# Kernel optimization log

Measured on AMD Instinct MI355X. Metric: run time of the kernel, lower is better.

Reference implementation:

```python
import jax, jax.numpy as jnp
import numpy as np

BN_EPS = 1e-5

def _l2norm(x):
    n = jnp.sqrt(jnp.sum(x * x, axis=-1, keepdims=True))
    return x / jnp.maximum(n, 1e-12)

def _bn_eval(x, gamma, beta):
    # eval-mode BatchNorm2d (running_mean=0, running_var=1)
    g = gamma / jnp.sqrt(1.0 + BN_EPS)
    return x * g[None, :, None, None] + beta[None, :, None, None]

def _forward(feat, Wq, Wk, Wv, ad_conv_w, ad_conv_b, pm_w1, pm_w2,
             back_w, catt, catt1, mlp_w, mlp_b, mlp_gamma, mlp_beta,
             dsn_w, dsn_b, dsn_gamma, dsn_beta):
    B, C, H, W = feat.shape
    p = pm_w1.shape[1]  # p_num (top-k size)
    x2d = feat.reshape(B, C, H * W).transpose(0, 2, 1)          # [B,HW,C]
    q = jnp.einsum('bnc,dc->bnd', x2d, Wq)                       # [B,HW,cim]
    k = jnp.einsum('bnc,dc->bnd', x2d, Wk)
    v = jnp.einsum('bnc,dc->bnd', x2d, Wv)
    # cosine-similarity attention weights [B,HW,HW]
    w = jnp.einsum('bid,bjd->bij', _l2norm(q), _l2norm(k))
    wv, idx = jax.lax.top_k(w, p)                                # [B,HW,p]
    vg = jax.vmap(lambda vv, ii: vv[ii])(v, idx)                 # [B,HW,p,cim] gather
    # ADConv: 1x1 conv on a single channel == scalar affine
    xa = wv * ad_conv_w[0] + ad_conv_b[0]
    pos = jnp.where(xa > 0, xa, 0.0)
    hdn = jax.nn.relu(jnp.einsum('bip,qp->biq', pos, pm_w1))     # [B,HW,2p]
    mask = jax.nn.sigmoid(jnp.einsum('biq,pq->bip', hdn, pm_w2)) # [B,HW,p]
    att = jax.nn.softmax(jnp.where(xa > 0, xa, -100000.0), axis=-1)
    wfin = att * mask                                            # [B,HW,p]
    ov = jnp.einsum('bip,bipd->bid', wfin, vg)                   # [B,HW,cim]
    ov = jnp.einsum('bid,cd->bic', ov, back_w)                   # [B,HW,C]
    v_img = catt * ov.transpose(0, 2, 1).reshape(B, C, H, W)
    cat = jnp.concatenate([v_img, catt1 * feat], axis=1)         # [B,2C,H,W]
    x = jnp.einsum('oc,bchw->bohw', mlp_w, cat) + mlp_b[None, :, None, None]
    x = jax.nn.relu(_bn_eval(x, mlp_gamma, mlp_beta))
    r0 = jnp.einsum('oc,bchw->bohw', dsn_w, x) + dsn_b[None, :, None, None]
    r0 = jax.nn.relu(_bn_eval(r0, dsn_gamma, dsn_beta))
    return x, r0

def setup_inputs() -> dict:
    key = jax.random.key(0)
    ks = jax.random.split(key, 12)
    B, C, H, W = 2, 256, 80, 80
    cim, p = C // 8, 9
    sc = 0.05
    return {
        'feat': jax.random.normal(ks[0], (B, C, H, W), jnp.float32),
        'Wq': jax.random.normal(ks[1], (cim, C), jnp.float32) * sc,
        'Wk': jax.random.normal(ks[2], (cim, C), jnp.float32) * sc,
        'Wv': jax.random.normal(ks[3], (cim, C), jnp.float32) * sc,
        'ad_conv_w': jnp.ones((1,), jnp.float32),
        'ad_conv_b': jnp.zeros((1,), jnp.float32),
        'pm_w1': jax.random.normal(ks[4], (2 * p, p), jnp.float32) * 0.3,
        'pm_w2': jax.random.normal(ks[5], (p, 2 * p), jnp.float32) * 0.3,
        'back_w': jax.random.normal(ks[6], (C, cim), jnp.float32) * sc,
        'catt': jnp.ones((1, C, 1, 1), jnp.float32),
        'catt1': jnp.ones((1, C, 1, 1), jnp.float32),
        'mlp_w': jax.random.normal(ks[7], (C, 2 * C), jnp.float32) * sc,
        'mlp_b': jnp.zeros((C,), jnp.float32),
        'mlp_gamma': jnp.ones((C,), jnp.float32),
        'mlp_beta': jnp.zeros((C,), jnp.float32),
        'dsn_w': jax.random.normal(ks[8], (1, C), jnp.float32) * sc,
        'dsn_b': jnp.zeros((1,), jnp.float32),
        'dsn_gamma': jnp.ones((1,), jnp.float32),
        'dsn_beta': jnp.zeros((1,), jnp.float32),
        'H': H,
        'W': W,
    }

def reference(feat, Wq, Wk, Wv, ad_conv_w, ad_conv_b, pm_w1, pm_w2,
              back_w, catt, catt1, mlp_w, mlp_b, mlp_gamma, mlp_beta,
              dsn_w, dsn_b, dsn_gamma, dsn_beta, H, W):
    # H,W < 768 -> get_forward branch
    return _forward(feat, Wq, Wk, Wv, ad_conv_w, ad_conv_b, pm_w1, pm_w2,
                    back_w, catt, catt1, mlp_w, mlp_b, mlp_gamma, mlp_beta,
                    dsn_w, dsn_b, dsn_gamma, dsn_beta)
```

## Files before the change

kernel.cpp:

```cpp
#include <hip/hip_runtime.h>
#include <hip/hip_bf16.h>

#define HW   6400
#define NB   2
#define CC   256
#define CIM  32
#define PP   9
#define P2   18
#define ROWS (NB*HW)
#define NCH  32
#define JCH  (HW/NCH)
#define NCHF 64
#define JCHF (HW/NCHF)
#define NGRP (ROWS/64)
#define CAPR 256

typedef float f4 __attribute__((ext_vector_type(4)));

#define OFF_QN   0
#define OFF_KN   (OFF_QN + ROWS*CIM)
#define OFF_V    (OFF_KN + ROWS*CIM)
#define OFF_OV   (OFF_V  + ROWS*CIM)
#define OFF_PV   (OFF_OV + ROWS*CIM)
#define OFF_PI   (OFF_PV + ROWS*NCH*PP)
#define OFF_W1T  (OFF_PI + ROWS*NCH*PP)
#define OFF_W2T  (OFF_W1T + CIM*CC)
#define OFF_BF   (OFF_W2T + CC*CC)
#define OFF_WQT  (OFF_BF + CC)
#define OFF_WKT  (OFF_WQT + CC*CIM)
#define OFF_WVT  (OFF_WKT + CC*CIM)
#define OFF_TH   (OFF_WVT + CC*CIM)
#define OFF_SC   (OFF_TH + ROWS)
#define OFF_SV   OFF_PV

__global__ void prep_kernel(const float* __restrict__ mlp_w, const float* __restrict__ mlp_b,
                            const float* __restrict__ mlp_g, const float* __restrict__ mlp_be,
                            const float* __restrict__ back_w, const float* __restrict__ catt,
                            const float* __restrict__ catt1,
                            const float* __restrict__ Wq, const float* __restrict__ Wk,
                            const float* __restrict__ Wv, float* __restrict__ ws) {
    const int blk = blockIdx.x, t = threadIdx.x;
    const float bnc = rsqrtf(1.0f + 1e-5f);
    if (blk < 32) {
        const int d = blk, o = t;
        const float g = mlp_g[o] * bnc;
        float acc = 0.f;
        for (int c = 0; c < CC; ++c)
            acc = fmaf(mlp_w[o*512 + c] * catt[c], back_w[c*CIM + d], acc);
        ws[OFF_W1T + d*CC + o] = g * acc;
    } else if (blk == 32) {
        const int o = t;
        const float g = mlp_g[o] * bnc;
        for (int c = 0; c < CC; ++c)
            ws[OFF_W2T + c*CC + o] = g * mlp_w[o*512 + 256 + c] * catt1[c];
        ws[OFF_BF + o] = g * mlp_b[o] + mlp_be[o];
    } else {
        const float* W = (blk == 33) ? Wq : (blk == 34) ? Wk : Wv;
        float* WT = ws + ((blk == 33) ? OFF_WQT : (blk == 34) ? OFF_WKT : OFF_WVT);
        for (int i = t; i < CC*CIM; i += 256) {
            const int c = i / CIM, d = i % CIM;
            WT[c*CIM + d] = W[d*CC + c];
        }
    }
}

__global__ __launch_bounds__(256) void qkv_kernel(const float* __restrict__ feat,
                                                  const float* __restrict__ ws_r,
                                                  float* __restrict__ ws) {
    __shared__ float part[4][64][33];
    __shared__ float invA[64];
    const int bx = blockIdx.x;
    const int mat = bx % 3;
    const int ng  = bx / 3;
    const int n0  = ng * 64;
    const int b   = n0 / HW;
    const int nsp0 = n0 % HW;
    const int tid = threadIdx.x;
    const int w = __builtin_amdgcn_readfirstlane(tid >> 6);
    const int lane = tid & 63;
    const float* WT = ws_r + (mat == 0 ? OFF_WQT : mat == 1 ? OFF_WKT : OFF_WVT);
    const float* fbase = feat + (size_t)b*CC*HW + nsp0 + lane;
    float acc[CIM];
#pragma unroll
    for (int d = 0; d < CIM; ++d) acc[d] = 0.f;
    const int c0 = w * 64;
    for (int cc = 0; cc < 64; cc += 2) {
        const int c = c0 + cc;
        const float fv0 = fbase[(size_t)c * HW];
        const float fv1 = fbase[(size_t)(c+1) * HW];
        const float* wt0 = WT + c*CIM;
        const float* wt1 = wt0 + CIM;
#pragma unroll
        for (int d = 0; d < CIM; ++d) acc[d] = fmaf(fv0, wt0[d], acc[d]);
#pragma unroll
        for (int d = 0; d < CIM; ++d) acc[d] = fmaf(fv1, wt1[d], acc[d]);
    }
#pragma unroll
    for (int d = 0; d < CIM; ++d) part[w][lane][d] = acc[d];
    __syncthreads();
    {
        const int n = tid >> 2, d0 = (tid & 3) * 8;
#pragma unroll
        for (int dd = 0; dd < 8; ++dd) {
            const int d = d0 + dd;
            part[0][n][d] = part[0][n][d] + part[1][n][d] + part[2][n][d] + part[3][n][d];
        }
    }
    __syncthreads();
    if (mat < 2) {
        if (tid < 64) {
            const int n = tid;
            float ss = 0.f;
#pragma unroll
            for (int d = 0; d < CIM; ++d) { const float x = part[0][n][d]; ss = fmaf(x, x, ss); }
            invA[n] = 1.0f / fmaxf(sqrtf(ss), 1e-12f);
        }
        __syncthreads();
    }
    float* outp = ws + (mat == 0 ? OFF_QN : mat == 1 ? OFF_KN : OFF_V);
    {
        const int n = tid >> 2, d0 = (tid & 3) * 8;
        const float scl = (mat < 2) ? invA[n] : 1.0f;
        const size_t r = (size_t)(n0 + n);
#pragma unroll
        for (int dd = 0; dd < 8; ++dd)
            outp[r*CIM + d0 + dd] = part[0][n][d0 + dd] * scl;
    }
}

__global__ __launch_bounds__(256) void attn_sample(const float* __restrict__ ws_r,
                                                   float* __restrict__ ws) {
    const int tid  = threadIdx.x;
    const int wid  = (blockIdx.x << 2) + (tid >> 6);
    const int lane = tid & 63;
    const int rg = __builtin_amdgcn_readfirstlane(wid >> 5);
    const int ch = __builtin_amdgcn_readfirstlane(wid & (NCH-1));
    const int r = rg*64 + lane;
    const int b = (rg*64) / HW;
    const float* qn = ws_r + OFF_QN + (size_t)r*CIM;
    float q[CIM];
    {   const f4* qv = (const f4*)qn;
        f4* q4 = (f4*)q;
#pragma unroll
        for (int h = 0; h < 8; ++h) q4[h] = qv[h];
    }
    const float* kbase = ws_r + OFF_KN + ((size_t)b*HW + ch*JCH)*CIM;
    const int jbase = ch*JCH;
    float tv[PP]; int ti[PP];
#pragma unroll
    for (int s = 0; s < PP; ++s) { tv[s] = -3.0e38f; ti[s] = 0; }
    for (int j = 0; j < JCH; j += 8) {
        const float* kp = kbase + j*CIM;
        float a0 = 0.f, a1 = 0.f, a2 = 0.f, a3 = 0.f;
#pragma unroll
        for (int d = 0; d < CIM; d += 4) {
            a0 = fmaf(q[d+0], kp[d+0], a0);
            a1 = fmaf(q[d+1], kp[d+1], a1);
            a2 = fmaf(q[d+2], kp[d+2], a2);
            a3 = fmaf(q[d+3], kp[d+3], a3);
        }
        const float wv = (a0 + a1) + (a2 + a3);
        if (wv > tv[8]) {
            tv[8] = wv; ti[8] = jbase + j;
#pragma unroll
            for (int s = 8; s > 0; --s) {
                const bool sw = tv[s] > tv[s-1];
                const float vA = tv[s-1], vB = tv[s];
                tv[s-1] = sw ? vB : vA;  tv[s] = sw ? vA : vB;
                const int iA = ti[s-1], iB = ti[s];
                ti[s-1] = sw ? iB : iA;  ti[s] = sw ? iA : iB;
            }
        }
    }
    float* pv = ws + OFF_PV + ((size_t)r*NCH + ch)*PP;
    int*   pi = (int*)(ws + OFF_PI) + ((size_t)r*NCH + ch)*PP;
#pragma unroll
    for (int s = 0; s < PP; ++s) { pv[s] = tv[s]; pi[s] = ti[s]; }
}

#define NSLOT 5
__global__ __launch_bounds__(256) void theta_kernel(const float* __restrict__ ws_r,
                                                    float* __restrict__ ws) {
    const int tid = threadIdx.x;
    const int w = tid >> 6, lane = tid & 63;
    const int r = blockIdx.x*4 + w;
    const float* pv = ws_r + OFF_PV + (size_t)r*NCH*PP;
    const int*   pi = (const int*)(ws_r + OFF_PI) + (size_t)r*NCH*PP;
    float cv[NSLOT]; int ci[NSLOT];
#pragma unroll
    for (int i = 0; i < NSLOT; ++i) {
        const int s = lane + 64*i;
        if (s < NCH*PP) { cv[i] = pv[s]; ci[i] = pi[s]; }
        else            { cv[i] = -3e38f; ci[i] = 0x7fffffff; }
    }
    float s9 = -3e38f;
#pragma unroll
    for (int rd = 0; rd < PP; ++rd) {
        float hv = cv[0]; int hi = ci[0]; int hs = 0;
#pragma unroll
        for (int i = 1; i < NSLOT; ++i)
            if (cv[i] > hv || (cv[i] == hv && ci[i] < hi)) { hv = cv[i]; hi = ci[i]; hs = i; }
        float bv = hv; int bi = hi;
#pragma unroll
        for (int off = 32; off >= 1; off >>= 1) {
            const float ov_ = __shfl_xor(bv, off);
            const int   oi_ = __shfl_xor(bi, off);
            if (ov_ > bv || (ov_ == bv && oi_ < bi)) { bv = ov_; bi = oi_; }
        }
        const bool won = (hv == bv && hi == bi);
#pragma unroll
        for (int i = 0; i < NSLOT; ++i)
            if (won && i == hs) cv[i] = -3e38f;
        s9 = bv;
    }
    if (lane == 0) {
        ws[OFF_TH + r] = s9;
        ((int*)(ws + OFF_SC))[r] = 0;
    }
}

__global__ __launch_bounds__(256) void attn_filter(const float* __restrict__ ws_r,
                                                   float* __restrict__ ws) {
    const int tid  = threadIdx.x;
    const int wid  = (blockIdx.x << 2) + (tid >> 6);
    const int lane = tid & 63;
    const int rg = __builtin_amdgcn_readfirstlane(wid >> 6);
    const int ch = __builtin_amdgcn_readfirstlane(wid & (NCHF-1));
    const int r = rg*64 + lane;
    const int b = (rg*64) / HW;
    const float* qn = ws_r + OFF_QN + (size_t)r*CIM;
    float q[CIM];
    {   const f4* qv = (const f4*)qn;
        f4* q4 = (f4*)q;
#pragma unroll
        for (int h = 0; h < 8; ++h) q4[h] = qv[h];
    }
    const float th = ws_r[OFF_TH + r];
    int* sc = (int*)(ws + OFF_SC);
    float* sv = ws + OFF_SV;
    const float* kbase = ws_r + OFF_KN + ((size_t)b*HW + ch*JCHF)*CIM;
    const int jbase = ch*JCHF;
#pragma unroll 2
    for (int j = 0; j < JCHF; ++j) {
        const float* kp = kbase + j*CIM;
        float a0 = 0.f, a1 = 0.f, a2 = 0.f, a3 = 0.f;
#pragma unroll
        for (int d = 0; d < CIM; d += 4) {
            a0 = fmaf(q[d+0], kp[d+0], a0);
            a1 = fmaf(q[d+1], kp[d+1], a1);
            a2 = fmaf(q[d+2], kp[d+2], a2);
            a3 = fmaf(q[d+3], kp[d+3], a3);
        }
        const float wv = (a0 + a1) + (a2 + a3);
        if (wv >= th) {
            const int slot = atomicAdd(&sc[r], 1);
            if (slot < CAPR) {
                float2 pr;
                pr.x = wv;
                pr.y = __int_as_float(jbase + j);
                *(float2*)(sv + ((size_t)r*CAPR + slot)*2) = pr;
            }
        }
    }
}

#define NS2 4
__global__ __launch_bounds__(256) void merge2_kernel(const float* __restrict__ ws_r,
                                                     const float* __restrict__ pm_w1,
                                                     const float* __restrict__ pm_w2,
                                                     const float* __restrict__ ad_w,
                                                     const float* __restrict__ ad_b,
                                                     float* __restrict__ ws) {
    __shared__ float pm1[P2*PP];
    __shared__ float pm2[PP*P2];
    const int tid = threadIdx.x;
    for (int i = tid; i < P2*PP; i += 256) pm1[i] = pm_w1[i];
    for (int i = tid; i < PP*P2; i += 256) pm2[i] = pm_w2[i];
    __syncthreads();
    const int w = tid >> 6, lane = tid & 63;
    const int r = blockIdx.x*4 + w;
    const int b = r / HW;
    const int cnt0 = ((const int*)(ws_r + OFF_SC))[r];
    const int cnl = cnt0 < CAPR ? cnt0 : CAPR;
    const float* svp = ws_r + OFF_SV + (size_t)r*CAPR*2;
    float cv[NS2]; int ci[NS2];
#pragma unroll
    for (int i = 0; i < NS2; ++i) {
        const int s = lane + 64*i;
        if (s < cnl) {
            const float2 pr = *(const float2*)(svp + (size_t)s*2);
            cv[i] = pr.x; ci[i] = __float_as_int(pr.y);
        } else { cv[i] = -3e38f; ci[i] = 0x7fffffff; }
    }
    float topv[PP]; int topi[PP];
#pragma unroll
    for (int rd = 0; rd < PP; ++rd) {
        float hv = cv[0]; int hi = ci[0]; int hs = 0;
#pragma unroll
        for (int i = 1; i < NS2; ++i)
            if (cv[i] > hv || (cv[i] == hv && ci[i] < hi)) { hv = cv[i]; hi = ci[i]; hs = i; }
        float bv = hv; int bi = hi;
#pragma unroll
        for (int off = 32; off >= 1; off >>= 1) {
            const float ov_ = __shfl_xor(bv, off);
            const int   oi_ = __shfl_xor(bi, off);
            if (ov_ > bv || (ov_ == bv && oi_ < bi)) { bv = ov_; bi = oi_; }
        }
        const bool won = (hv == bv && hi == bi);
#pragma unroll
        for (int i = 0; i < NS2; ++i)
            if (won && i == hs) cv[i] = -3e38f;
        topv[rd] = bv;
        topi[rd] = (bi >= 0 && bi < HW) ? bi : 0;
    }
    const float adw = ad_w[0], adb = ad_b[0];
    float xa[PP], pos[PP];
#pragma unroll
    for (int p = 0; p < PP; ++p) { xa[p] = fmaf(topv[p], adw, adb); pos[p] = fmaxf(xa[p], 0.f); }
    float hdn[P2];
#pragma unroll
    for (int qq = 0; qq < P2; ++qq) {
        float a = 0.f;
#pragma unroll
        for (int p = 0; p < PP; ++p) a = fmaf(pos[p], pm1[qq*PP + p], a);
        hdn[qq] = fmaxf(a, 0.f);
    }
    float msk[PP];
#pragma unroll
    for (int p = 0; p < PP; ++p) {
        float a = 0.f;
#pragma unroll
        for (int qq = 0; qq < P2; ++qq) a = fmaf(hdn[qq], pm2[p*P2 + qq], a);
        msk[p] = 1.0f / (1.0f + expf(-a));
    }
    float xm[PP], m = -3e38f;
#pragma unroll
    for (int p = 0; p < PP; ++p) { xm[p] = xa[p] > 0.f ? xa[p] : -100000.0f; m = fmaxf(m, xm[p]); }
    float e[PP], ssum = 0.f;
#pragma unroll
    for (int p = 0; p < PP; ++p) { e[p] = expf(xm[p] - m); ssum += e[p]; }
    float wf[PP];
#pragma unroll
    for (int p = 0; p < PP; ++p) wf[p] = (e[p] / ssum) * msk[p];
    const int d = lane & 31;
    const float* vb = ws_r + OFF_V + (size_t)b*HW*CIM;
    float acc = 0.f;
#pragma unroll
    for (int p = 0; p < PP; ++p) acc = fmaf(wf[p], vb[(size_t)topi[p]*CIM + d], acc);
    if (lane < 32) ws[OFF_OV + (size_t)r*CIM + d] = acc;
}

__global__ __launch_bounds__(64) void fin_kernel(const float* __restrict__ feat,
                                                 const float* __restrict__ ws_r,
                                                 float* __restrict__ out) {
    __shared__ float ovt[64*33];
    const int bx = blockIdx.x;
    const int ng = bx % NGRP;
    const int og = bx / NGRP;
    const int n0 = ng*64;
    const int b  = n0 / HW;
    const int nsp0 = n0 % HW;
    const int lane = threadIdx.x;
    const float4* ovg = (const float4*)(ws_r + OFF_OV + (size_t)n0*CIM);
#pragma unroll
    for (int i = 0; i < 8; ++i) {
        const int f = lane + 64*i;
        const float4 vv = ovg[f];
        const int row = f >> 3, col = (f & 7) * 4;
        ovt[row*33 + col]     = vv.x;
        ovt[row*33 + col + 1] = vv.y;
        ovt[row*33 + col + 2] = vv.z;
        ovt[row*33 + col + 3] = vv.w;
    }
    __syncthreads();
    const int o0 = og * 16;
    float acc[16];
    const float* bfp = ws_r + OFF_BF;
#pragma unroll
    for (int oi = 0; oi < 16; ++oi) acc[oi] = bfp[o0 + oi];
    const float* w1t = ws_r + OFF_W1T;
    for (int dd = 0; dd < CIM; dd += 4) {
        const float xv0 = ovt[lane*33 + dd+0];
        const float xv1 = ovt[lane*33 + dd+1];
        const float xv2 = ovt[lane*33 + dd+2];
        const float xv3 = ovt[lane*33 + dd+3];
        const float* w0 = w1t + (dd+0)*CC + o0;
        const float* w1 = w1t + (dd+1)*CC + o0;
        const float* w2 = w1t + (dd+2)*CC + o0;
        const float* w3 = w1t + (dd+3)*CC + o0;
#pragma unroll
        for (int oi = 0; oi < 16; ++oi) acc[oi] = fmaf(xv0, w0[oi], acc[oi]);
#pragma unroll
        for (int oi = 0; oi < 16; ++oi) acc[oi] = fmaf(xv1, w1[oi], acc[oi]);
#pragma unroll
        for (int oi = 0; oi < 16; ++oi) acc[oi] = fmaf(xv2, w2[oi], acc[oi]);
#pragma unroll
        for (int oi = 0; oi < 16; ++oi) acc[oi] = fmaf(xv3, w3[oi], acc[oi]);
    }
    const float* w2t = ws_r + OFF_W2T;
    const float* fbase = feat + (size_t)b*CC*HW + nsp0 + lane;
    for (int c = 0; c < CC; c += 4) {
        const float fv0 = fbase[(size_t)(c+0) * HW];
        const float fv1 = fbase[(size_t)(c+1) * HW];
        const float fv2 = fbase[(size_t)(c+2) * HW];
        const float fv3 = fbase[(size_t)(c+3) * HW];
        const float* w0 = w2t + (c+0)*CC + o0;
        const float* w1 = w2t + (c+1)*CC + o0;
        const float* w2 = w2t + (c+2)*CC + o0;
        const float* w3 = w2t + (c+3)*CC + o0;
#pragma unroll
        for (int oi = 0; oi < 16; ++oi) acc[oi] = fmaf(fv0, w0[oi], acc[oi]);
#pragma unroll
        for (int oi = 0; oi < 16; ++oi) acc[oi] = fmaf(fv1, w1[oi], acc[oi]);
#pragma unroll
        for (int oi = 0; oi < 16; ++oi) acc[oi] = fmaf(fv2, w2[oi], acc[oi]);
#pragma unroll
        for (int oi = 0; oi < 16; ++oi) acc[oi] = fmaf(fv3, w3[oi], acc[oi]);
    }
    const size_t obase = (size_t)b*CC*HW + nsp0 + lane;
#pragma unroll
    for (int oi = 0; oi < 16; ++oi)
        out[obase + (size_t)(o0 + oi)*HW] = fmaxf(acc[oi], 0.f);
}

__global__ __launch_bounds__(256) void dsn_kernel(const float* __restrict__ xout,
                                                  const float* __restrict__ dsn_w,
                                                  const float* __restrict__ dsn_b,
                                                  const float* __restrict__ dsn_g,
                                                  const float* __restrict__ dsn_be,
                                                  float* __restrict__ out) {
    const int t = blockIdx.x*256 + threadIdx.x;
    const int b = t / HW, nsp = t % HW;
    const float* xb = xout + (size_t)b*CC*HW + nsp;
    float acc = 0.f;
#pragma unroll 4
    for (int o = 0; o < CC; ++o)
        acc = fmaf(xb[(size_t)o*HW], dsn_w[o], acc);
    const float g = dsn_g[0] * rsqrtf(1.0f + 1e-5f);
    const float r0 = fmaxf(fmaf(g, acc + dsn_b[0], dsn_be[0]), 0.f);
    out[(size_t)NB*CC*HW + t] = r0;
}

extern "C" void kernel_launch(void* const* d_in, const int* in_sizes, int n_in,
                              void* d_out, int out_size, void* d_ws, size_t ws_size,
                              hipStream_t stream) {
    const float* feat  = (const float*)d_in[0];
    const float* Wq    = (const float*)d_in[1];
    const float* Wk    = (const float*)d_in[2];
    const float* Wv    = (const float*)d_in[3];
    const float* adw   = (const float*)d_in[4];
    const float* adb   = (const float*)d_in[5];
    const float* pm_w1 = (const float*)d_in[6];
    const float* pm_w2 = (const float*)d_in[7];
    const float* backw = (const float*)d_in[8];
    const float* catt  = (const float*)d_in[9];
    const float* catt1 = (const float*)d_in[10];
    const float* mlp_w = (const float*)d_in[11];
    const float* mlp_b = (const float*)d_in[12];
    const float* mlp_g = (const float*)d_in[13];
    const float* mlp_be= (const float*)d_in[14];
    const float* dsn_w = (const float*)d_in[15];
    const float* dsn_b = (const float*)d_in[16];
    const float* dsn_g = (const float*)d_in[17];
    const float* dsn_be= (const float*)d_in[18];
    float* ws = (float*)d_ws;
    float* out = (float*)d_out;

    prep_kernel<<<36, 256, 0, stream>>>(mlp_w, mlp_b, mlp_g, mlp_be, backw, catt, catt1,
                                        Wq, Wk, Wv, ws);
    qkv_kernel<<<NGRP*3, 256, 0, stream>>>(feat, ws, ws);
    attn_sample<<<(NGRP*NCH)/4, 256, 0, stream>>>(ws, ws);
    theta_kernel<<<ROWS/4, 256, 0, stream>>>(ws, ws);
    attn_filter<<<(NGRP*NCHF)/4, 256, 0, stream>>>(ws, ws);
    merge2_kernel<<<ROWS/4, 256, 0, stream>>>(ws, pm_w1, pm_w2, adw, adb, ws);
    fin_kernel<<<NGRP*16, 64, 0, stream>>>(feat, ws, out);
    dsn_kernel<<<ROWS/256, 256, 0, stream>>>(out, dsn_w, dsn_b, dsn_g, dsn_be, out);
}
```

Before: 298.0 us.

## Filter top-k candidates with bf16 MFMA and recompute exact scores in merge

The fp32 scalar full similarity pass used to filter top-k candidates is replaced by a bf16 MFMA 16x16x32 pass. It keeps candidate indices whose approximate score exceeds the sampled threshold minus a tolerance. The merge kernel then recomputes exact fp32 dot products for the surviving candidates, so final selection stays exact as long as the tolerance covers bf16 error. In exchange the qkv kernel writes extra bf16 copies of q and k, the looser threshold lets in more candidates and more atomics, and the per-row candidate cap of 256 could overflow.

After: 305.2 us. 2.4% more time.

```diff
diff --git a/kernel.cpp b/kernel.cpp
--- a/kernel.cpp
+++ b/kernel.cpp
@@ -10,12 +10,13 @@
 #define ROWS (NB*HW)
 #define NCH  32
 #define JCH  (HW/NCH)
-#define NCHF 64
-#define JCHF (HW/NCHF)
 #define NGRP (ROWS/64)
 #define CAPR 256
+#define WEPS 1.0e-2f
 
 typedef float f4 __attribute__((ext_vector_type(4)));
+typedef short s8v __attribute__((ext_vector_type(8)));
+typedef float f4v __attribute__((ext_vector_type(4)));
 
 #define OFF_QN   0
 #define OFF_KN   (OFF_QN + ROWS*CIM)
@@ -32,6 +33,14 @@
 #define OFF_TH   (OFF_WVT + CC*CIM)
 #define OFF_SC   (OFF_TH + ROWS)
 #define OFF_SV   OFF_PV
+#define OFF_Q16  OFF_OV
+#define OFF_K16  (OFF_OV + ROWS*CIM/2)
+
+__device__ __forceinline__ unsigned short f2bf(float x) {
+    union { __hip_bfloat16 h; unsigned short u; } cv;
+    cv.h = __float2bfloat16(x);
+    return cv.u;
+}
 
 __global__ void prep_kernel(const float* __restrict__ mlp_w, const float* __restrict__ mlp_b,
                             const float* __restrict__ mlp_g, const float* __restrict__ mlp_be,
@@ -118,13 +127,17 @@
         __syncthreads();
     }
     float* outp = ws + (mat == 0 ? OFF_QN : mat == 1 ? OFF_KN : OFF_V);
+    unsigned short* o16 = (unsigned short*)(ws + (mat == 0 ? OFF_Q16 : OFF_K16));
     {
         const int n = tid >> 2, d0 = (tid & 3) * 8;
         const float scl = (mat < 2) ? invA[n] : 1.0f;
         const size_t r = (size_t)(n0 + n);
 #pragma unroll
-        for (int dd = 0; dd < 8; ++dd)
-            outp[r*CIM + d0 + dd] = part[0][n][d0 + dd] * scl;
+        for (int dd = 0; dd < 8; ++dd) {
+            const float v = part[0][n][d0 + dd] * scl;
+            outp[r*CIM + d0 + dd] = v;
+            if (mat < 2) o16[r*CIM + d0 + dd] = f2bf(v);
+        }
     }
 }
 
@@ -219,46 +232,49 @@
     }
 }
 
-__global__ __launch_bounds__(256) void attn_filter(const float* __restrict__ ws_r,
-                                                   float* __restrict__ ws) {
-    const int tid  = threadIdx.x;
-    const int wid  = (blockIdx.x << 2) + (tid >> 6);
+__global__ __launch_bounds__(256) void attn_mfma(const float* __restrict__ ws_r,
+                                                 float* __restrict__ ws) {
+    const int tid = threadIdx.x;
+    const int w = __builtin_amdgcn_readfirstlane(tid >> 6);
     const int lane = tid & 63;
-    const int rg = __builtin_amdgcn_readfirstlane(wid >> 6);
-    const int ch = __builtin_amdgcn_readfirstlane(wid & (NCHF-1));
-    const int r = rg*64 + lane;
-    const int b = (rg*64) / HW;
-    const float* qn = ws_r + OFF_QN + (size_t)r*CIM;
-    float q[CIM];
-    {   const f4* qv = (const f4*)qn;
-        f4* q4 = (f4*)q;
-#pragma unroll
-        for (int h = 0; h < 8; ++h) q4[h] = qv[h];
-    }
-    const float th = ws_r[OFF_TH + r];
+    const int bx = blockIdx.x;
+    const int rg = bx / 25;
+    const int jg = bx % 25;
+    const int b  = (rg*64) / HW;
+    const int l15 = lane & 15, lhi = lane >> 4;
+    const unsigned short* q16 = (const unsigned short*)(ws_r + OFF_Q16);
+    const unsigned short* k16 = (const unsigned short*)(ws_r + OFF_K16) + (size_t)b*HW*CIM;
+    s8v afr[4];
+#pragma unroll
+    for (int rt = 0; rt < 4; ++rt) {
+        const int row = rg*64 + rt*16 + l15;
+        afr[rt] = *(const s8v*)(q16 + (size_t)row*CIM + lhi*8);
+    }
+    float th4[4][4];
+#pragma unroll
+    for (int rt = 0; rt < 4; ++rt)
+#pragma unroll
+        for (int r = 0; r < 4; ++r)
+            th4[rt][r] = ws_r[OFF_TH + rg*64 + rt*16 + lhi*4 + r] - WEPS;
     int* sc = (int*)(ws + OFF_SC);
-    float* sv = ws + OFF_SV;
-    const float* kbase = ws_r + OFF_KN + ((size_t)b*HW + ch*JCHF)*CIM;
-    const int jbase = ch*JCHF;
-#pragma unroll 2
-    for (int j = 0; j < JCHF; ++j) {
-        const float* kp = kbase + j*CIM;
-        float a0 = 0.f, a1 = 0.f, a2 = 0.f, a3 = 0.f;
-#pragma unroll
-        for (int d = 0; d < CIM; d += 4) {
-            a0 = fmaf(q[d+0], kp[d+0], a0);
-            a1 = fmaf(q[d+1], kp[d+1], a1);
-            a2 = fmaf(q[d+2], kp[d+2], a2);
-            a3 = fmaf(q[d+3], kp[d+3], a3);
-        }
-        const float wv = (a0 + a1) + (a2 + a3);
-        if (wv >= th) {
-            const int slot = atomicAdd(&sc[r], 1);
-            if (slot < CAPR) {
-                float2 pr;
-                pr.x = wv;
-                pr.y = __int_as_float(jbase + j);
-                *(float2*)(sv + ((size_t)r*CAPR + slot)*2) = pr;
+    int* si = (int*)(ws + OFF_SV);
+    const int j0 = jg*256 + w*64;
+#pragma unroll
+    for (int jt = 0; jt < 4; ++jt) {
+        const int jcol0 = j0 + jt*16;
+        const s8v bfr = *(const s8v*)(k16 + (size_t)(jcol0 + l15)*CIM + lhi*8);
+        const int jj = jcol0 + l15;
+#pragma unroll
+        for (int rt = 0; rt < 4; ++rt) {
+            f4v acc = {0.f, 0.f, 0.f, 0.f};
+            acc = __builtin_amdgcn_mfma_f32_16x16x32_bf16(afr[rt], bfr, acc, 0, 0, 0);
+#pragma unroll
+            for (int r = 0; r < 4; ++r) {
+                if (acc[r] >= th4[rt][r]) {
+                    const int row = rg*64 + rt*16 + lhi*4 + r;
+                    const int slot = atomicAdd(&sc[row], 1);
+                    if (slot < CAPR) si[(size_t)row*CAPR + slot] = jj;
+                }
             }
         }
     }
@@ -277,19 +293,33 @@
     for (int i = tid; i < P2*PP; i += 256) pm1[i] = pm_w1[i];
     for (int i = tid; i < PP*P2; i += 256) pm2[i] = pm_w2[i];
     __syncthreads();
-    const int w = tid >> 6, lane = tid & 63;
+    const int w = __builtin_amdgcn_readfirstlane(tid >> 6);
+    const int lane = tid & 63;
     const int r = blockIdx.x*4 + w;
     const int b = r / HW;
     const int cnt0 = ((const int*)(ws_r + OFF_SC))[r];
     const int cnl = cnt0 < CAPR ? cnt0 : CAPR;
-    const float* svp = ws_r + OFF_SV + (size_t)r*CAPR*2;
+    const int* sip = (const int*)(ws_r + OFF_SV) + (size_t)r*CAPR;
+    const float* qp = ws_r + OFF_QN + (size_t)r*CIM;
+    const float* kb = ws_r + OFF_KN + (size_t)b*HW*CIM;
     float cv[NS2]; int ci[NS2];
 #pragma unroll
     for (int i = 0; i < NS2; ++i) {
         const int s = lane + 64*i;
         if (s < cnl) {
-            const float2 pr = *(const float2*)(svp + (size_t)s*2);
-            cv[i] = pr.x; ci[i] = __float_as_int(pr.y);
+            const int jj = sip[s];
+            const int jc = (jj >= 0 && jj < HW) ? jj : 0;
+            const float* kp = kb + (size_t)jc*CIM;
+            float a0 = 0.f, a1 = 0.f, a2 = 0.f, a3 = 0.f;
+#pragma unroll
+            for (int d = 0; d < CIM; d += 4) {
+                a0 = fmaf(qp[d+0], kp[d+0], a0);
+                a1 = fmaf(qp[d+1], kp[d+1], a1);
+                a2 = fmaf(qp[d+2], kp[d+2], a2);
+                a3 = fmaf(qp[d+3], kp[d+3], a3);
+            }
+            cv[i] = (a0 + a1) + (a2 + a3);
+            ci[i] = jc;
         } else { cv[i] = -3e38f; ci[i] = 0x7fffffff; }
     }
     float topv[PP]; int topi[PP];
@@ -471,7 +501,7 @@
     qkv_kernel<<<NGRP*3, 256, 0, stream>>>(feat, ws, ws);
     attn_sample<<<(NGRP*NCH)/4, 256, 0, stream>>>(ws, ws);
     theta_kernel<<<ROWS/4, 256, 0, stream>>>(ws, ws);
-    attn_filter<<<(NGRP*NCHF)/4, 256, 0, stream>>>(ws, ws);
+    attn_mfma<<<NGRP*25, 256, 0, stream>>>(ws, ws);
     merge2_kernel<<<ROWS/4, 256, 0, stream>>>(ws, pm_w1, pm_w2, adw, adb, ws);
     fin_kernel<<<NGRP*16, 64, 0, stream>>>(feat, ws, out);
     dsn_kernel<<<ROWS/256, 256, 0, stream>>>(out, dsn_w, dsn_b, dsn_g, dsn_be, out);
```
